# Kernel optimization log

Hardware: AMD Instinct MI355X
Metric: run time of the kernel (lower is better)

## Reference

```python
import jax, jax.numpy as jnp
import numpy as np


def setup_inputs() -> dict:
    key = jax.random.key(0)
    k1, k2, k3, k4 = jax.random.split(key, 4)
    b, c, h, w = 4, 256, 64, 64
    Fq_l = jax.random.normal(k1, (b, c, h, w), dtype=jnp.float32)
    Fp_l = jax.random.normal(k2, (b, c, h, w), dtype=jnp.float32)
    # 1x1 conv: weight [out=c//2, in=c], bias [c//2]
    W = jax.random.normal(k3, (c // 2, c), dtype=jnp.float32) * (1.0 / np.sqrt(c))
    bias = jax.random.normal(k4, (c // 2,), dtype=jnp.float32) * 0.01
    return {"Fq_l": Fq_l, "Fp_l": Fp_l, "W": W, "bias": bias}


def reference(Fq_l, Fp_l, W, bias):
    b, c, h, w = Fq_l.shape
    hw = h * w
    # 1x1 conv == per-pixel linear projection
    q = jnp.einsum('oc,bchw->bohw', W, Fq_l) + bias[None, :, None, None]
    p = jnp.einsum('oc,bchw->bohw', W, Fp_l) + bias[None, :, None, None]
    qf = q.reshape(b, -1, hw)  # [b, c/2, hw]
    pf = p.reshape(b, -1, hw)
    qf = qf / jnp.linalg.norm(qf, axis=1, keepdims=True)
    pf = pf / jnp.linalg.norm(pf, axis=1, keepdims=True)
    # cosine similarity, [b, hw, hw]
    sim = jnp.einsum('bcn,bcm->bnm', qf, pf)
    idx = jnp.argmax(sim, axis=-1)  # [b, hw]
    Fp_flat = Fp_l.reshape(b, c, hw)
    aligned = jnp.take_along_axis(Fp_flat, idx[:, None, :], axis=2)  # [b, c, hw]
    return aligned.reshape(b, c, h, w)
```

## Files before the change

kernel.cpp:

```cpp
#include <hip/hip_runtime.h>

#define HW 4096
#define LCAP 1536

typedef short bf16x8 __attribute__((ext_vector_type(8)));
typedef float f32x16 __attribute__((ext_vector_type(16)));

__device__ __forceinline__ ushort f2bf_rne(float f) {
    unsigned u = __float_as_uint(f);
    return (ushort)((u + 0x7FFFu + ((u >> 16) & 1u)) >> 16);
}

__global__ __launch_bounds__(256) void transpose_w_kernel(
    const float* __restrict__ Wm, float* __restrict__ Wt)
{
    const int o = blockIdx.x;
    const int c = threadIdx.x;
    Wt[c * 128 + o] = Wm[o * 256 + c];
}

__global__ __launch_bounds__(256) void proj_kernel(
    const float* __restrict__ Fq, const float* __restrict__ Fp,
    const float* __restrict__ Wt, const float* __restrict__ bias,
    float* __restrict__ Qt, float* __restrict__ Pt,
    ushort* __restrict__ Qpk, ushort* __restrict__ Ppk)
{
    __shared__ float Ws[64][128];
    __shared__ float Xs[64][64];
    __shared__ float psum[16][68];

    const int tid = threadIdx.x;
    const int z  = blockIdx.z;
    const float* __restrict__ X = z ? Fp : Fq;
    const int b  = blockIdx.y;
    const int n0 = blockIdx.x * 64;
    const int og = tid >> 4;
    const int ng = tid & 15;

    float acc[4][8];
    #pragma unroll
    for (int i = 0; i < 4; ++i)
        #pragma unroll
        for (int j = 0; j < 8; ++j) acc[i][j] = 0.f;

    float4 w0, w1, w2, w3, w4, w5, w6, w7;
    float4 x0, x1, x2, x3;
    const int xr0 = tid >> 4,            xn0 = (tid & 15) * 4;
    const int xr1 = (256 + tid) >> 4,    xn1 = xn0;
    const int xr2 = (512 + tid) >> 4,    xn2 = xn0;
    const int xr3 = (768 + tid) >> 4,    xn3 = xn0;

#define LOAD_CHUNK(cc_)                                                        \
    {                                                                          \
        const float4* s_ = (const float4*)(Wt + (size_t)(cc_) * 64 * 128);     \
        w0 = s_[0 * 256 + tid]; w1 = s_[1 * 256 + tid];                        \
        w2 = s_[2 * 256 + tid]; w3 = s_[3 * 256 + tid];                        \
        w4 = s_[4 * 256 + tid]; w5 = s_[5 * 256 + tid];                        \
        w6 = s_[6 * 256 + tid]; w7 = s_[7 * 256 + tid];                        \
        const size_t cb_ = (size_t)(b * 256 + (cc_) * 64);                     \
        x0 = *(const float4*)&X[(cb_ + xr0) * HW + n0 + xn0];                  \
        x1 = *(const float4*)&X[(cb_ + xr1) * HW + n0 + xn1];                  \
        x2 = *(const float4*)&X[(cb_ + xr2) * HW + n0 + xn2];                  \
        x3 = *(const float4*)&X[(cb_ + xr3) * HW + n0 + xn3];                  \
    }

    LOAD_CHUNK(0);

    for (int cc = 0; cc < 4; ++cc) {
        __syncthreads();
        {
            float4* dst = (float4*)Ws;
            dst[0 * 256 + tid] = w0; dst[1 * 256 + tid] = w1;
            dst[2 * 256 + tid] = w2; dst[3 * 256 + tid] = w3;
            dst[4 * 256 + tid] = w4; dst[5 * 256 + tid] = w5;
            dst[6 * 256 + tid] = w6; dst[7 * 256 + tid] = w7;
        }
        *(float4*)&Xs[xr0][xn0] = x0;
        *(float4*)&Xs[xr1][xn1] = x1;
        *(float4*)&Xs[xr2][xn2] = x2;
        *(float4*)&Xs[xr3][xn3] = x3;
        __syncthreads();

        if (cc < 3) LOAD_CHUNK(cc + 1);

        for (int r = 0; r < 64; ++r) {
            float4 a0 = *(const float4*)&Ws[r][og * 8];
            float4 a1 = *(const float4*)&Ws[r][og * 8 + 4];
            float4 xv = *(const float4*)&Xs[r][ng * 4];
            float wa[8] = {a0.x, a0.y, a0.z, a0.w, a1.x, a1.y, a1.z, a1.w};
            float xa[4] = {xv.x, xv.y, xv.z, xv.w};
            #pragma unroll
            for (int i = 0; i < 4; ++i)
                #pragma unroll
                for (int j = 0; j < 8; ++j)
                    acc[i][j] += wa[j] * xa[i];
        }
    }
#undef LOAD_CHUNK

    {
        float4 b0 = *(const float4*)&bias[og * 8];
        float4 b1 = *(const float4*)&bias[og * 8 + 4];
        float ba[8] = {b0.x, b0.y, b0.z, b0.w, b1.x, b1.y, b1.z, b1.w};
        #pragma unroll
        for (int i = 0; i < 4; ++i)
            #pragma unroll
            for (int j = 0; j < 8; ++j) acc[i][j] += ba[j];
    }

    #pragma unroll
    for (int i = 0; i < 4; ++i) {
        float s = 0.f;
        #pragma unroll
        for (int j = 0; j < 8; ++j) s += acc[i][j] * acc[i][j];
        psum[og][ng * 4 + i] = s;
    }
    __syncthreads();
    float tot[4];
    #pragma unroll
    for (int i = 0; i < 4; ++i) {
        float s = 0.f;
        #pragma unroll
        for (int g = 0; g < 16; ++g) s += psum[g][ng * 4 + i];
        tot[i] = s;
    }

    float pscale[4];
    if (z) {
        #pragma unroll
        for (int i = 0; i < 4; ++i) {
            float s = 1.0f / sqrtf(tot[i]);
            #pragma unroll
            for (int j = 0; j < 8; ++j) acc[i][j] *= s;
            pscale[i] = 1.0f;
        }
    } else {
        #pragma unroll
        for (int i = 0; i < 4; ++i) pscale[i] = 256.0f / sqrtf(tot[i]);
    }

    {
        float* __restrict__ T = z ? Pt : Qt;
        #pragma unroll
        for (int i = 0; i < 4; ++i) {
            size_t tb = ((size_t)b * HW + n0 + ng * 4 + i) * 128 + og * 8;
            *(float4*)&T[tb]     = make_float4(acc[i][0], acc[i][1], acc[i][2], acc[i][3]);
            *(float4*)&T[tb + 4] = make_float4(acc[i][4], acc[i][5], acc[i][6], acc[i][7]);
        }
    }
    {
        ushort* __restrict__ PK = z ? Ppk : Qpk;
        const int ks = og >> 1;
        #pragma unroll
        for (int i = 0; i < 4; ++i) {
            const int na  = n0 + ng * 4 + i;
            const int t32 = na >> 5;
            const int lt  = (na & 31) + 32 * (og & 1);
            ushort u[8];
            #pragma unroll
            for (int k = 0; k < 8; ++k) u[k] = f2bf_rne(acc[i][k] * pscale[i]);
            size_t pk = ((((size_t)b * 128 + t32) * 8 + ks) * 64 + lt) * 8;
            uint4 w;
            w.x = (unsigned)u[0] | ((unsigned)u[1] << 16);
            w.y = (unsigned)u[2] | ((unsigned)u[3] << 16);
            w.z = (unsigned)u[4] | ((unsigned)u[5] << 16);
            w.w = (unsigned)u[6] | ((unsigned)u[7] << 16);
            *(uint4*)&PK[pk] = w;
        }
    }
}

__global__ __launch_bounds__(256, 4) void sim_sketch_kernel(
    const ushort* __restrict__ Qpk, const ushort* __restrict__ Ppk,
    unsigned char* __restrict__ SK, unsigned char* __restrict__ BM)
{
    __shared__ ushort Bs[16384];

    const int tid  = threadIdx.x;
    const int lane = tid & 63;
    const int w    = tid >> 6;
    const int nb   = blockIdx.x;
    const int b    = blockIdx.y;
    const int ms   = blockIdx.z;
    const int hi   = lane >> 5;

    {
        const uint4* src = (const uint4*)(Ppk + ((size_t)(b * 128 + ms * 4)) * 4096);
        uint4* dst = (uint4*)Bs;
        #pragma unroll
        for (int it = 0; it < 8; ++it) dst[it * 256 + tid] = src[it * 256 + tid];
    }

    const ushort* __restrict__ qbase =
        Qpk + ((size_t)(b * 128 + nb * 4)) * 4096 + (size_t)lane * 8;
    bf16x8 qf[8];
    #pragma unroll
    for (int ks = 0; ks < 8; ++ks)
        qf[ks] = *(const bf16x8*)(qbase + (w * 8 + ks) * 512);

    const size_t g16f = (size_t)b * 256 + (size_t)(nb * 4 + w) * 2 + hi;
    const int mb0 = ms * 128 + (lane & 31);

    float xmax[16];
    #pragma unroll
    for (int r = 0; r < 16; ++r) xmax[r] = -1e30f;

    __syncthreads();

    #pragma unroll 2
    for (int mtl = 0; mtl < 4; ++mtl) {
        f32x16 acc;
        #pragma unroll
        for (int r = 0; r < 16; ++r) acc[r] = 0.f;
        #pragma unroll
        for (int ks = 0; ks < 8; ++ks) {
            bf16x8 bb = *(const bf16x8*)&Bs[((mtl * 8 + ks) * 64 + lane) * 8];
            acc = __builtin_amdgcn_mfma_f32_32x32x16_bf16(qf[ks], bb, acc, 0, 0, 0);
        }

        unsigned dw[4] = {0u, 0u, 0u, 0u};
        #pragma unroll
        for (int r = 0; r < 16; ++r) {
            float x = acc[r];
            xmax[r] = fmaxf(xmax[r], x);
#if __has_builtin(__builtin_amdgcn_cvt_pk_u8_f32)
            dw[r >> 2] = (unsigned)__builtin_amdgcn_cvt_pk_u8_f32(
                x, (unsigned)(r & 3), (int)dw[r >> 2]);
#else
            int vi = (int)rintf(x);
            vi = vi < 0 ? 0 : (vi > 255 ? 255 : vi);
            dw[r >> 2] |= (unsigned)vi << (8 * (r & 3));
#endif
        }
        const int m = mb0 + mtl * 32;
        uint4 pk;
        pk.x = dw[0]; pk.y = dw[1]; pk.z = dw[2]; pk.w = dw[3];
        *(uint4*)(SK + ((g16f * 4096 + (size_t)m) << 4)) = pk;
    }

    #pragma unroll
    for (int r = 0; r < 16; ++r) {
        float v = xmax[r];
        #pragma unroll
        for (int d = 1; d < 32; d <<= 1)
            v = fmaxf(v, __shfl_xor(v, d, 64));
        xmax[r] = v;
    }
    if ((lane & 31) == 0) {
        unsigned dw[4] = {0u, 0u, 0u, 0u};
        #pragma unroll
        for (int r = 0; r < 16; ++r) {
#if __has_builtin(__builtin_amdgcn_cvt_pk_u8_f32)
            dw[r >> 2] = (unsigned)__builtin_amdgcn_cvt_pk_u8_f32(
                xmax[r], (unsigned)(r & 3), (int)dw[r >> 2]);
#else
            int vi = (int)rintf(xmax[r]);
            vi = vi < 0 ? 0 : (vi > 255 ? 255 : vi);
            dw[r >> 2] |= (unsigned)vi << (8 * (r & 3));
#endif
        }
        uint4 pk;
        pk.x = dw[0]; pk.y = dw[1]; pk.z = dw[2]; pk.w = dw[3];
        *(uint4*)(BM + ((g16f * 32 + (size_t)ms) << 4)) = pk;
    }
}

__device__ __noinline__ void dot_one_slow(
    const float* Qsrow, const float* __restrict__ Pt,
    int b, int m, int n, unsigned long long* __restrict__ best)
{
    const float4* __restrict__ pr = (const float4*)&Pt[((size_t)b * HW + m) * 128];
    float acc = 0.f;
    #pragma unroll
    for (int k = 0; k < 32; ++k) {
        float4 pv = pr[k];
        float4 qv = *(const float4*)&Qsrow[k * 4];
        acc += qv.x * pv.x + qv.y * pv.y + qv.z * pv.z + qv.w * pv.w;
    }
    unsigned u = __float_as_uint(acc);
    unsigned kk = (u & 0x80000000u) ? ~u : (u | 0x80000000u);
    unsigned long long key = ((unsigned long long)kk << 32) | (unsigned)(4095 - m);
    atomicMax(&best[(size_t)b * HW + n], key);
}

__global__ __launch_bounds__(256) void scan_rescore_kernel(
    const unsigned char* __restrict__ SK, const unsigned char* __restrict__ BM,
    const float* __restrict__ Qt, const float* __restrict__ Pt,
    unsigned long long* __restrict__ best)
{
    __shared__ float Qs[16][132];
    __shared__ int nlist[16];
    __shared__ int t8s[16];
    __shared__ ushort hl[LCAP];
    __shared__ unsigned lcnt;

    const int fg  = blockIdx.x;
    const int tid = threadIdx.x;
    const int b = fg >> 8, g = fg & 255, t = g >> 1, gs = g & 1;

    if (tid == 0) lcnt = 0u;
    if (tid < 16) {
        int n = t * 32 + (tid & 3) + 8 * (tid >> 2) + 4 * gs;
        nlist[tid] = n;
        best[(size_t)b * HW + n] = 0ull;
        const unsigned char* __restrict__ bmrow = BM + ((size_t)fg << 9);
        int mc = 0;
        #pragma unroll
        for (int ms = 0; ms < 32; ++ms)
            mc = max(mc, (int)bmrow[ms * 16 + tid]);
        int tt = mc - 6;
        t8s[tid] = tt < 0 ? 0 : tt;
    }
    __syncthreads();

    #pragma unroll
    for (int it = 0; it < 2; ++it) {
        int idx = it * 256 + tid;
        int row = idx >> 5, c4 = (idx & 31) * 4;
        *(float4*)&Qs[row][c4] =
            *(const float4*)&Qt[((size_t)b * HW + nlist[row]) * 128 + c4];
    }

    int myt[16];
    #pragma unroll
    for (int j = 0; j < 16; ++j) myt[j] = t8s[j];
    unsigned tw[4];
    #pragma unroll
    for (int d = 0; d < 4; ++d)
        tw[d] = (unsigned)myt[d * 4]
              | ((unsigned)myt[d * 4 + 1] << 8)
              | ((unsigned)myt[d * 4 + 2] << 16)
              | ((unsigned)myt[d * 4 + 3] << 24);
    __syncthreads();

    const uint4* __restrict__ skrow = (const uint4*)(SK + ((size_t)fg << 16));
    const unsigned H = 0x80808080u;

    #pragma unroll 4
    for (int it = 0; it < 16; ++it) {
        const int m = it * 256 + tid;
        uint4 v = skrow[it * 256 + tid];
        unsigned wv[4] = {v.x, v.y, v.z, v.w};
        unsigned ge[4];
        #pragma unroll
        for (int d = 0; d < 4; ++d) {
            unsigned x = wv[d], y = tw[d];
            unsigned L = (x | H) - (y & ~H);
            ge[d] = ((x & ~y) | (~(x ^ y) & L)) & H;
        }
        if (ge[0] | ge[1] | ge[2] | ge[3]) {
            #pragma unroll
            for (int d = 0; d < 4; ++d) {
                if (ge[d]) {
                    #pragma unroll
                    for (int k = 0; k < 4; ++k) {
                        if (ge[d] & (0x80u << (8 * k))) {
                            int j = d * 4 + k;
                            unsigned pos = atomicAdd(&lcnt, 1u);
                            if (pos < LCAP) {
                                hl[pos] = (ushort)((j << 12) | m);
                            } else {
                                dot_one_slow(&Qs[j][0], Pt, b, m, nlist[j], best);
                            }
                        }
                    }
                }
            }
        }
    }

    __syncthreads();
    unsigned cnt = lcnt < LCAP ? lcnt : LCAP;
    for (unsigned p = tid; p < cnt; p += 256) {
        int e = hl[p];
        int j = e >> 12, m = e & 4095;
        const float4* __restrict__ pr = (const float4*)&Pt[((size_t)b * HW + m) * 128];
        float acc = 0.f;
        #pragma unroll
        for (int k = 0; k < 32; ++k) {
            float4 pv = pr[k];
            float4 qv = *(const float4*)&Qs[j][k * 4];
            acc += qv.x * pv.x + qv.y * pv.y + qv.z * pv.z + qv.w * pv.w;
        }
        unsigned u = __float_as_uint(acc);
        unsigned kk = (u & 0x80000000u) ? ~u : (u | 0x80000000u);
        unsigned long long key = ((unsigned long long)kk << 32) | (unsigned)(4095 - m);
        atomicMax(&best[(size_t)b * HW + nlist[j]], key);
    }
}

__global__ __launch_bounds__(256) void gather_kernel(
    const float* __restrict__ Fp, const unsigned long long* __restrict__ best,
    float* __restrict__ out)
{
    __shared__ float row[4096];
    const int blk = blockIdx.x;
    const int c = blk & 255;
    const int b = blk >> 8;
    const int tid = threadIdx.x;

    const float* __restrict__ src = Fp + ((size_t)b * 256 + c) * HW;
    #pragma unroll
    for (int it = 0; it < 4; ++it) {
        int f = it * 256 + tid;
        *(float4*)&row[f * 4] = *(const float4*)&src[f * 4];
    }
    __syncthreads();

    float* __restrict__ dst = out + ((size_t)b * 256 + c) * HW;
    #pragma unroll
    for (int it = 0; it < 16; ++it) {
        int n = it * 256 + tid;
        int m = 4095 - (int)(best[(size_t)b * HW + n] & 0xFFFull);
        dst[n] = row[m];
    }
}

extern "C" void kernel_launch(void* const* d_in, const int* in_sizes, int n_in,
                              void* d_out, int out_size, void* d_ws, size_t ws_size,
                              hipStream_t stream) {
    const float* Fq   = (const float*)d_in[0];
    const float* Fp   = (const float*)d_in[1];
    const float* Wm   = (const float*)d_in[2];
    const float* bias = (const float*)d_in[3];
    float* out = (float*)d_out;

    char* base = (char*)d_ws;
    float*  Qt    = (float*)(base);
    float*  Pt    = (float*)(base + (8u << 20));
    ushort* Qpk   = (ushort*)(base + (16u << 20));
    ushort* Ppk   = (ushort*)(base + (20u << 20));
    unsigned char* SK = (unsigned char*)(base + (24u << 20));
    char* x = base + (88u << 20);
    unsigned char* BM = (unsigned char*)x;  x += 524288;
    unsigned long long* best = (unsigned long long*)x; x += 131072;
    float*  Wtg   = (float*)x;

    transpose_w_kernel<<<128, 256, 0, stream>>>(Wm, Wtg);
    proj_kernel<<<dim3(64, 4, 2), 256, 0, stream>>>(Fq, Fp, Wtg, bias,
                                                    Qt, Pt, Qpk, Ppk);
    sim_sketch_kernel<<<dim3(32, 4, 32), 256, 0, stream>>>(Qpk, Ppk, SK, BM);
    scan_rescore_kernel<<<1024, 256, 0, stream>>>(SK, BM, Qt, Pt, best);
    gather_kernel<<<1024, 256, 0, stream>>>(Fp, best, out);
}
```

Baseline: 170.5 us.

## Emit sparse candidate lists from sim kernel instead of full 8-bit sketch

The sim kernel no longer writes the full 64 MB quantized similarity sketch. It filters candidates in-block against a local per-tile max threshold and appends them to per-query-group global candidate lists, with an overflow buffer. The rescore kernel then reads only those candidates and applies the final global threshold. This removes the large sketch write and scan traffic. In exchange it adds shared and global atomics, and the overflow path is a linear scan of the whole overflow buffer by every block.

```diff
diff --git a/kernel.cpp b/kernel.cpp
--- a/kernel.cpp
+++ b/kernel.cpp
@@ -1,7 +1,9 @@
 #include <hip/hip_runtime.h>
 
 #define HW 4096
-#define LCAP 1536
+#define LBCAP 192u
+#define GCAP  4096u
+#define OCAP  2097152u
 
 typedef short bf16x8 __attribute__((ext_vector_type(8)));
 typedef float f32x16 __attribute__((ext_vector_type(16)));
@@ -12,11 +14,17 @@
 }
 
 __global__ __launch_bounds__(256) void transpose_w_kernel(
-    const float* __restrict__ Wm, float* __restrict__ Wt)
+    const float* __restrict__ Wm, float* __restrict__ Wt,
+    unsigned* __restrict__ gcnt, unsigned* __restrict__ ocnt)
 {
     const int o = blockIdx.x;
     const int c = threadIdx.x;
     Wt[c * 128 + o] = Wm[o * 256 + c];
+    if (o == 0) {
+        #pragma unroll
+        for (int i = 0; i < 4; ++i) gcnt[i * 256 + c] = 0u;
+        if (c == 0) ocnt[0] = 0u;
+    }
 }
 
 __global__ __launch_bounds__(256) void proj_kernel(
@@ -170,11 +178,16 @@
     }
 }
 
-__global__ __launch_bounds__(256, 4) void sim_sketch_kernel(
+__global__ __launch_bounds__(256, 4) void sim_emit_kernel(
     const ushort* __restrict__ Qpk, const ushort* __restrict__ Ppk,
-    unsigned char* __restrict__ SK, unsigned char* __restrict__ BM)
+    unsigned char* __restrict__ BM,
+    unsigned* __restrict__ cand, unsigned* __restrict__ gcnt,
+    unsigned long long* __restrict__ ocand, unsigned* __restrict__ ocnt)
 {
     __shared__ ushort Bs[16384];
+    __shared__ unsigned llist[8][LBCAP];
+    __shared__ unsigned lcnt[8];
+    __shared__ unsigned lbase[8];
 
     const int tid  = threadIdx.x;
     const int lane = tid & 63;
@@ -184,6 +197,8 @@
     const int ms   = blockIdx.z;
     const int hi   = lane >> 5;
 
+    if (tid < 8) lcnt[tid] = 0u;
+
     {
         const uint4* src = (const uint4*)(Ppk + ((size_t)(b * 128 + ms * 4)) * 4096);
         uint4* dst = (uint4*)Bs;
@@ -199,11 +214,14 @@
         qf[ks] = *(const bf16x8*)(qbase + (w * 8 + ks) * 512);
 
     const size_t g16f = (size_t)b * 256 + (size_t)(nb * 4 + w) * 2 + hi;
+    const int g16l = w * 2 + hi;
     const int mb0 = ms * 128 + (lane & 31);
 
     float xmax[16];
     #pragma unroll
     for (int r = 0; r < 16; ++r) xmax[r] = -1e30f;
+
+    uint4 cds[4];
 
     __syncthreads();
 
@@ -232,10 +250,8 @@
             dw[r >> 2] |= (unsigned)vi << (8 * (r & 3));
 #endif
         }
-        const int m = mb0 + mtl * 32;
-        uint4 pk;
-        pk.x = dw[0]; pk.y = dw[1]; pk.z = dw[2]; pk.w = dw[3];
-        *(uint4*)(SK + ((g16f * 4096 + (size_t)m) << 4)) = pk;
+        cds[mtl].x = dw[0]; cds[mtl].y = dw[1];
+        cds[mtl].z = dw[2]; cds[mtl].w = dw[3];
     }
 
     #pragma unroll
@@ -263,42 +279,91 @@
         pk.x = dw[0]; pk.y = dw[1]; pk.z = dw[2]; pk.w = dw[3];
         *(uint4*)(BM + ((g16f * 32 + (size_t)ms) << 4)) = pk;
     }
-}
-
-__device__ __noinline__ void dot_one_slow(
-    const float* Qsrow, const float* __restrict__ Pt,
-    int b, int m, int n, unsigned long long* __restrict__ best)
-{
-    const float4* __restrict__ pr = (const float4*)&Pt[((size_t)b * HW + m) * 128];
-    float acc = 0.f;
-    #pragma unroll
-    for (int k = 0; k < 32; ++k) {
-        float4 pv = pr[k];
-        float4 qv = *(const float4*)&Qsrow[k * 4];
-        acc += qv.x * pv.x + qv.y * pv.y + qv.z * pv.z + qv.w * pv.w;
-    }
-    unsigned u = __float_as_uint(acc);
-    unsigned kk = (u & 0x80000000u) ? ~u : (u | 0x80000000u);
-    unsigned long long key = ((unsigned long long)kk << 32) | (unsigned)(4095 - m);
-    atomicMax(&best[(size_t)b * HW + n], key);
+
+    unsigned tw[4];
+    #pragma unroll
+    for (int d = 0; d < 4; ++d) tw[d] = 0u;
+    #pragma unroll
+    for (int r = 0; r < 16; ++r) {
+        int vi = (int)rintf(xmax[r]);
+        vi = vi < 0 ? 0 : (vi > 255 ? 255 : vi);
+        vi -= 7;
+        if (vi < 0) vi = 0;
+        tw[r >> 2] |= (unsigned)vi << (8 * (r & 3));
+    }
+
+    const unsigned H = 0x80808080u;
+    #pragma unroll
+    for (int mtl = 0; mtl < 4; ++mtl) {
+        unsigned wv[4] = {cds[mtl].x, cds[mtl].y, cds[mtl].z, cds[mtl].w};
+        const int m = mb0 + mtl * 32;
+        #pragma unroll
+        for (int d = 0; d < 4; ++d) {
+            unsigned x = wv[d], y = tw[d];
+            unsigned L = (x | H) - (y & ~H);
+            unsigned ge = ((x & ~y) | (~(x ^ y) & L)) & H;
+            if (ge) {
+                #pragma unroll
+                for (int k = 0; k < 4; ++k) {
+                    if (ge & (0x80u << (8 * k))) {
+                        int j = d * 4 + k;
+                        unsigned code = (x >> (8 * k)) & 255u;
+                        unsigned e = (code << 24) | ((unsigned)j << 20) | (unsigned)m;
+                        unsigned pos = atomicAdd(&lcnt[g16l], 1u);
+                        if (pos < LBCAP) {
+                            llist[g16l][pos] = e;
+                        } else {
+                            unsigned op = atomicAdd(ocnt, 1u);
+                            if (op < OCAP)
+                                ocand[op] = ((unsigned long long)g16f << 32) | e;
+                        }
+                    }
+                }
+            }
+        }
+    }
+
+    __syncthreads();
+    if (tid < 8) {
+        unsigned c = lcnt[tid];
+        if (c > LBCAP) c = LBCAP;
+        lcnt[tid] = c;
+        size_t fgo = (size_t)b * 256 + (size_t)(nb * 4 + (tid >> 1)) * 2 + (tid & 1);
+        lbase[tid] = atomicAdd(&gcnt[fgo], c);
+    }
+    __syncthreads();
+    #pragma unroll 1
+    for (int gl = 0; gl < 8; ++gl) {
+        unsigned c = lcnt[gl], base = lbase[gl];
+        size_t fgo = (size_t)b * 256 + (size_t)(nb * 4 + (gl >> 1)) * 2 + (gl & 1);
+        for (unsigned i = tid; i < c; i += 256) {
+            unsigned dst = base + i;
+            if (dst < GCAP) {
+                cand[fgo * GCAP + dst] = llist[gl][i];
+            } else {
+                unsigned op = atomicAdd(ocnt, 1u);
+                if (op < OCAP)
+                    ocand[op] = ((unsigned long long)fgo << 32) | llist[gl][i];
+            }
+        }
+    }
 }
 
 __global__ __launch_bounds__(256) void scan_rescore_kernel(
-    const unsigned char* __restrict__ SK, const unsigned char* __restrict__ BM,
+    const unsigned char* __restrict__ BM,
+    const unsigned* __restrict__ cand, const unsigned* __restrict__ gcnt,
+    const unsigned long long* __restrict__ ocand, const unsigned* __restrict__ ocnt,
     const float* __restrict__ Qt, const float* __restrict__ Pt,
     unsigned long long* __restrict__ best)
 {
     __shared__ float Qs[16][132];
     __shared__ int nlist[16];
     __shared__ int t8s[16];
-    __shared__ ushort hl[LCAP];
-    __shared__ unsigned lcnt;
 
     const int fg  = blockIdx.x;
     const int tid = threadIdx.x;
     const int b = fg >> 8, g = fg & 255, t = g >> 1, gs = g & 1;
 
-    if (tid == 0) lcnt = 0u;
     if (tid < 16) {
         int n = t * 32 + (tid & 3) + 8 * (tid >> 2) + 4 * gs;
         nlist[tid] = n;
@@ -320,72 +385,50 @@
         *(float4*)&Qs[row][c4] =
             *(const float4*)&Qt[((size_t)b * HW + nlist[row]) * 128 + c4];
     }
-
-    int myt[16];
-    #pragma unroll
-    for (int j = 0; j < 16; ++j) myt[j] = t8s[j];
-    unsigned tw[4];
-    #pragma unroll
-    for (int d = 0; d < 4; ++d)
-        tw[d] = (unsigned)myt[d * 4]
-              | ((unsigned)myt[d * 4 + 1] << 8)
-              | ((unsigned)myt[d * 4 + 2] << 16)
-              | ((unsigned)myt[d * 4 + 3] << 24);
-    __syncthreads();
-
-    const uint4* __restrict__ skrow = (const uint4*)(SK + ((size_t)fg << 16));
-    const unsigned H = 0x80808080u;
-
-    #pragma unroll 4
-    for (int it = 0; it < 16; ++it) {
-        const int m = it * 256 + tid;
-        uint4 v = skrow[it * 256 + tid];
-        unsigned wv[4] = {v.x, v.y, v.z, v.w};
-        unsigned ge[4];
-        #pragma unroll
-        for (int d = 0; d < 4; ++d) {
-            unsigned x = wv[d], y = tw[d];
-            unsigned L = (x | H) - (y & ~H);
-            ge[d] = ((x & ~y) | (~(x ^ y) & L)) & H;
-        }
-        if (ge[0] | ge[1] | ge[2] | ge[3]) {
-            #pragma unroll
-            for (int d = 0; d < 4; ++d) {
-                if (ge[d]) {
-                    #pragma unroll
-                    for (int k = 0; k < 4; ++k) {
-                        if (ge[d] & (0x80u << (8 * k))) {
-                            int j = d * 4 + k;
-                            unsigned pos = atomicAdd(&lcnt, 1u);
-                            if (pos < LCAP) {
-                                hl[pos] = (ushort)((j << 12) | m);
-                            } else {
-                                dot_one_slow(&Qs[j][0], Pt, b, m, nlist[j], best);
-                            }
-                        }
-                    }
-                }
+    __syncthreads();
+
+    unsigned cnt = gcnt[fg];
+    if (cnt > GCAP) cnt = GCAP;
+    for (unsigned p = tid; p < cnt; p += 256) {
+        unsigned e = cand[(size_t)fg * GCAP + p];
+        int code = (int)(e >> 24), j = (int)((e >> 20) & 15u), m = (int)(e & 4095u);
+        if (code >= t8s[j]) {
+            const float4* __restrict__ pr = (const float4*)&Pt[((size_t)b * HW + m) * 128];
+            float acc = 0.f;
+            #pragma unroll
+            for (int k = 0; k < 32; ++k) {
+                float4 pv = pr[k];
+                float4 qv = *(const float4*)&Qs[j][k * 4];
+                acc += qv.x * pv.x + qv.y * pv.y + qv.z * pv.z + qv.w * pv.w;
             }
-        }
-    }
-
-    __syncthreads();
-    unsigned cnt = lcnt < LCAP ? lcnt : LCAP;
-    for (unsigned p = tid; p < cnt; p += 256) {
-        int e = hl[p];
-        int j = e >> 12, m = e & 4095;
-        const float4* __restrict__ pr = (const float4*)&Pt[((size_t)b * HW + m) * 128];
-        float acc = 0.f;
-        #pragma unroll
-        for (int k = 0; k < 32; ++k) {
-            float4 pv = pr[k];
-            float4 qv = *(const float4*)&Qs[j][k * 4];
-            acc += qv.x * pv.x + qv.y * pv.y + qv.z * pv.z + qv.w * pv.w;
-        }
-        unsigned u = __float_as_uint(acc);
-        unsigned kk = (u & 0x80000000u) ? ~u : (u | 0x80000000u);
-        unsigned long long key = ((unsigned long long)kk << 32) | (unsigned)(4095 - m);
-        atomicMax(&best[(size_t)b * HW + nlist[j]], key);
+            unsigned u = __float_as_uint(acc);
+            unsigned kk = (u & 0x80000000u) ? ~u : (u | 0x80000000u);
+            unsigned long long key = ((unsigned long long)kk << 32) | (unsigned)(4095 - m);
+            atomicMax(&best[(size_t)b * HW + nlist[j]], key);
+        }
+    }
+
+    unsigned total = ocnt[0];
+    if (total > OCAP) total = OCAP;
+    for (unsigned p = tid; p < total; p += 256) {
+        unsigned long long ee = ocand[p];
+        if ((int)(ee >> 32) != fg) continue;
+        unsigned e = (unsigned)ee;
+        int code = (int)(e >> 24), j = (int)((e >> 20) & 15u), m = (int)(e & 4095u);
+        if (code >= t8s[j]) {
+            const float4* __restrict__ pr = (const float4*)&Pt[((size_t)b * HW + m) * 128];
+            float acc = 0.f;
+            #pragma unroll
+            for (int k = 0; k < 32; ++k) {
+                float4 pv = pr[k];
+                float4 qv = *(const float4*)&Qs[j][k * 4];
+                acc += qv.x * pv.x + qv.y * pv.y + qv.z * pv.z + qv.w * pv.w;
+            }
+            unsigned u = __float_as_uint(acc);
+            unsigned kk = (u & 0x80000000u) ? ~u : (u | 0x80000000u);
+            unsigned long long key = ((unsigned long long)kk << 32) | (unsigned)(4095 - m);
+            atomicMax(&best[(size_t)b * HW + nlist[j]], key);
+        }
     }
 }
 
@@ -430,16 +473,21 @@
     float*  Pt    = (float*)(base + (8u << 20));
     ushort* Qpk   = (ushort*)(base + (16u << 20));
     ushort* Ppk   = (ushort*)(base + (20u << 20));
-    unsigned char* SK = (unsigned char*)(base + (24u << 20));
-    char* x = base + (88u << 20);
+    unsigned* cand = (unsigned*)(base + (24u << 20));
+    unsigned long long* ocand = (unsigned long long*)(base + (40u << 20));
+    char* x = base + (56u << 20);
     unsigned char* BM = (unsigned char*)x;  x += 524288;
+    unsigned* gcnt = (unsigned*)x;          x += 4096;
+    unsigned* ocnt = (unsigned*)x;          x += 4096;
     unsigned long long* best = (unsigned long long*)x; x += 131072;
     float*  Wtg   = (float*)x;
 
-    transpose_w_kernel<<<128, 256, 0, stream>>>(Wm, Wtg);
+    transpose_w_kernel<<<128, 256, 0, stream>>>(Wm, Wtg, gcnt, ocnt);
     proj_kernel<<<dim3(64, 4, 2), 256, 0, stream>>>(Fq, Fp, Wtg, bias,
                                                     Qt, Pt, Qpk, Ppk);
-    sim_sketch_kernel<<<dim3(32, 4, 32), 256, 0, stream>>>(Qpk, Ppk, SK, BM);
-    scan_rescore_kernel<<<1024, 256, 0, stream>>>(SK, BM, Qt, Pt, best);
+    sim_emit_kernel<<<dim3(32, 4, 32), 256, 0, stream>>>(Qpk, Ppk, BM,
+                                                         cand, gcnt, ocand, ocnt);
+    scan_rescore_kernel<<<1024, 256, 0, stream>>>(BM, cand, gcnt, ocand, ocnt,
+                                                  Qt, Pt, best);
     gather_kernel<<<1024, 256, 0, stream>>>(Fp, best, out);
 }
```

Measured after the change: 202.1 us. +18.6%, slower.
